# Kernel optimization log

Measured on AMD Instinct MI355X. Metric: run time of the kernel, lower is better.

The kernel has to match this reference:

```python
import jax, jax.numpy as jnp
import numpy as np

ROPE_BASE = 10000.0

def _rope_tables(T, head_dim, dtype):
    inv_freq = 1.0 / (ROPE_BASE ** (jnp.arange(0, head_dim, 2, dtype=jnp.float32) / head_dim))
    freqs = jnp.arange(T, dtype=jnp.float32)[:, None] * inv_freq[None, :]  # (T, hd/2)
    freqs = jnp.repeat(freqs, 2, axis=-1)  # (T, hd) interleaved (lucidrains-style)
    return jnp.cos(freqs).astype(dtype), jnp.sin(freqs).astype(dtype)

def _rotate_half(x):
    # interleaved pairs: (..., d) -> (-x2, x1) interleaved
    x = x.reshape(x.shape[:-1] + (-1, 2))
    x1, x2 = x[..., 0], x[..., 1]
    return jnp.stack((-x2, x1), axis=-1).reshape(x.shape[:-2] + (-1,))

def _apply_rope(x, cos, sin):
    # x: (B, H, T, hd); cos/sin: (T, hd)
    return x * cos[None, None] + _rotate_half(x) * sin[None, None]

def setup_inputs() -> dict:
    key = jax.random.key(0)
    k1, k2, k3 = jax.random.split(key, 3)
    B, T, C = 4, 2048, 1024
    x = jax.random.normal(k1, (B, T, C), dtype=jnp.float32)
    W_attn = jax.random.normal(k2, (C, 3 * C), dtype=jnp.float32) * 0.02
    W_proj = jax.random.normal(k3, (C, C), dtype=jnp.float32) * 0.02
    return {"x": x, "W_attn": W_attn, "W_proj": W_proj}

def reference(x, W_attn, W_proj):
    B, T, C = x.shape
    n_head = 16
    hd = C // n_head
    qkv = x @ W_attn  # (B, T, 3C)
    q, k, v = jnp.split(qkv, 3, axis=-1)
    # (B, T, H, hd) -> (B, H, T, hd)
    q = q.reshape(B, T, n_head, hd).transpose(0, 2, 1, 3)
    k = k.reshape(B, T, n_head, hd).transpose(0, 2, 1, 3)
    v = v.reshape(B, T, n_head, hd).transpose(0, 2, 1, 3)
    cos, sin = _rope_tables(T, hd, x.dtype)
    q = _apply_rope(q, cos, sin)
    k = _apply_rope(k, cos, sin)
    att = jnp.einsum('bhqd,bhkd->bhqk', q, k) * (1.0 / jnp.sqrt(jnp.array(hd, dtype=x.dtype)))
    causal = jnp.tril(jnp.ones((T, T), dtype=bool))
    att = jnp.where(causal[None, None], att, jnp.array(-jnp.inf, dtype=att.dtype))
    att = jax.nn.softmax(att, axis=-1)
    y = jnp.einsum('bhqk,bhkd->bhqd', att, v)
    y = y.transpose(0, 2, 1, 3).reshape(B, T, C)
    return y @ W_proj
```

## Files before the change

kernel.cpp:

```cpp
#include <hip/hip_runtime.h>
#include <hip/hip_bf16.h>
#include <math.h>

#define BB 4
#define TT 2048
#define CC 1024
#define NH 16
#define HD 64
#define C3 3072
#define LDK 72

#define QSCALE 0.18033688011112042f

typedef __attribute__((ext_vector_type(8))) short bf16x8;
typedef __attribute__((ext_vector_type(4))) float f32x4;

__device__ __forceinline__ void gload_lds16(const __hip_bfloat16* g, __hip_bfloat16* s) {
    __builtin_amdgcn_global_load_lds((const __attribute__((address_space(1))) void*)g,
                                     (__attribute__((address_space(3))) void*)s, 16, 0, 0);
}

__global__ __launch_bounds__(256) void rope_tables(float2* __restrict__ tab) {
    int idx = blockIdx.x * 256 + threadIdx.x;
    int t = idx >> 5;
    int p = idx & 31;
    float invf = exp2f((float)p * (-13.287712379549449f / 32.0f));
    float ang = (float)t * invf;
    float s, c;
    sincosf(ang, &s, &c);
    tab[idx] = make_float2(c, s);
}

__global__ __launch_bounds__(256) void cast_bf16x8(const float* __restrict__ X,
                                                   __hip_bfloat16* __restrict__ Y) {
    size_t i = ((size_t)blockIdx.x * 256 + threadIdx.x) * 8;
    float4 a = *(const float4*)(X + i);
    float4 b = *(const float4*)(X + i + 4);
    __align__(16) __hip_bfloat16 tmp[8];
    tmp[0] = __float2bfloat16(a.x);
    tmp[1] = __float2bfloat16(a.y);
    tmp[2] = __float2bfloat16(a.z);
    tmp[3] = __float2bfloat16(a.w);
    tmp[4] = __float2bfloat16(b.x);
    tmp[5] = __float2bfloat16(b.y);
    tmp[6] = __float2bfloat16(b.z);
    tmp[7] = __float2bfloat16(b.w);
    *(bf16x8*)(Y + i) = *(bf16x8*)tmp;
}

__global__ __launch_bounds__(256) void wtrans(const float* __restrict__ W,
                                              __hip_bfloat16* __restrict__ Wt,
                                              int K, int N) {
    __shared__ float st[64][65];
    const int n0 = blockIdx.x * 64;
    const int k0 = blockIdx.y * 64;
    const int tid = threadIdx.x;
    const int r = tid >> 4;
    const int c4 = (tid & 15) * 4;
#pragma unroll
    for (int p = 0; p < 4; ++p) {
        int k = p * 16 + r;
        float4 v = *(const float4*)(W + (size_t)(k0 + k) * N + n0 + c4);
        st[c4 + 0][k] = v.x;
        st[c4 + 1][k] = v.y;
        st[c4 + 2][k] = v.z;
        st[c4 + 3][k] = v.w;
    }
    __syncthreads();
    const int rr = tid >> 3;
    const int cc = (tid & 7) * 8;
#pragma unroll
    for (int p = 0; p < 2; ++p) {
        int n = p * 32 + rr;
        __align__(16) __hip_bfloat16 tmp[8];
#pragma unroll
        for (int j = 0; j < 8; ++j) tmp[j] = __float2bfloat16(st[n][cc + j]);
        *(bf16x8*)(Wt + (size_t)(n0 + n) * K + k0 + cc) = *(bf16x8*)tmp;
    }
}

#define CA0 0
#define CA1 1
#define CB0 2
#define CB1 3

#define BAR() __builtin_amdgcn_s_barrier()
#define SB0() __builtin_amdgcn_sched_barrier(0)
#define WAIT_LGKM0() do { asm volatile("s_waitcnt lgkmcnt(0)" ::: "memory"); SB0(); } while (0)
#define WAIT_VM4()   do { asm volatile("s_waitcnt vmcnt(4)" ::: "memory");  SB0(); } while (0)

#define CLAMP_TS(x) ((x) < NTILE ? (x) : (x) - 2)

#define STAGE(gbase, h, ts, buf, cid) do {                                            \
    const __hip_bfloat16* _s = (gbase) + (size_t)((h) * 128 + w * 16) * K + (ts) * 64; \
    __hip_bfloat16* _d = &lds[buf][cid][w * 1024];                                    \
    gload_lds16(_s, _d);                                                              \
    gload_lds16(_s + 32, _d + 512);                                                   \
} while (0)

#define FRAGP(buf, cid, rowsub, ks)                                                   \
    ((const bf16x8*)((const char*)&lds[buf][cid][0] +                                 \
        (((rowsub) * 2 + (ks)) << 10) + (l16 << 6) + swzoff))

#define READ_A(buf, mi) do {                                                          \
    _Pragma("unroll") for (int _m = 0; _m < 4; ++_m)                                  \
    _Pragma("unroll") for (int _k = 0; _k < 2; ++_k)                                  \
        af[_m][_k] = *FRAGP(buf, wm, (mi) * 4 + _m, _k);                              \
} while (0)

#define READ_B(buf, ni) do {                                                          \
    _Pragma("unroll") for (int _n = 0; _n < 2; ++_n)                                  \
    _Pragma("unroll") for (int _k = 0; _k < 2; ++_k)                                  \
        bfr[(ni) * 2 + _n][_k] =                                                      \
            *FRAGP(buf, 2 + (wn >> 1), (wn & 1) * 4 + (ni) * 2 + _n, _k);             \
} while (0)

#define MFMA_Q(mb, nb) do {                                                           \
    __builtin_amdgcn_s_setprio(1);                                                    \
    _Pragma("unroll") for (int _m = 0; _m < 4; ++_m)                                  \
    _Pragma("unroll") for (int _n = 0; _n < 2; ++_n)                                  \
    _Pragma("unroll") for (int _k = 0; _k < 2; ++_k)                                  \
        acc[(mb) * 4 + _m][(nb) * 2 + _n] = __builtin_amdgcn_mfma_f32_16x16x32_bf16(  \
            af[_m][_k], bfr[(nb) * 2 + _n][_k], acc[(mb) * 4 + _m][(nb) * 2 + _n],    \
            0, 0, 0);                                                                 \
    __builtin_amdgcn_s_setprio(0);                                                    \
} while (0)

#define HALF_ITER(BUF, T12, B12, T34, B34) do {                                       \
                                                                 \
    READ_A(BUF, 0);                                                                   \
    READ_B(BUF, 0);                                                                   \
    STAGE(Bb, 1, CLAMP_TS(T12), B12, CB1);                                            \
    BAR(); WAIT_LGKM0();                                                              \
    MFMA_Q(0, 0);                                                                     \
    BAR();                                                                            \
                                                                 \
    READ_B(BUF, 1);                                                                   \
    STAGE(Ab, 1, CLAMP_TS(T12), B12, CA1);                                            \
    BAR(); WAIT_LGKM0();                                                              \
    MFMA_Q(0, 1);                                                                     \
    BAR();                                                                            \
                                                                 \
    READ_A(BUF, 1);                                                                   \
    STAGE(Bb, 0, CLAMP_TS(T34), B34, CB0);                                            \
    BAR(); WAIT_LGKM0();                                                              \
    MFMA_Q(1, 0);                                                                     \
    BAR();                                                                            \
                                                                 \
    STAGE(Ab, 0, CLAMP_TS(T34), B34, CA0);                                            \
    BAR(); WAIT_LGKM0();                                                              \
    MFMA_Q(1, 1);                                                                     \
    WAIT_VM4();                                                                       \
    BAR(); SB0();                                                                     \
} while (0)

#define GEMM256_BODY                                                                  \
    __shared__ __align__(16) __hip_bfloat16 lds[2][4][8192];             \
    const int tid = threadIdx.x;                                                      \
    const int w = tid >> 6;                                                           \
    const int lane = tid & 63;                                                        \
    const int l16 = lane & 15;                                                        \
    const int quad = lane >> 4;                                                       \
    const int wm = w >> 2;                                                            \
    const int wn = w & 3;                                                             \
    const int swzoff = ((quad * 8) ^ ((l16 & 8) << 1)) << 1;                          \
    const int bm0 = blockIdx.y * 256;                                                 \
    const int bn0 = blockIdx.x * 256;                                                 \
    const int NTILE = K >> 6;                                                         \
    const size_t laneOff = (size_t)(lane >> 2) * K +                                  \
                           (((lane & 3) * 8) ^ ((lane >> 5) << 4));                   \
    const __hip_bfloat16* Ab = A + (size_t)bm0 * K + laneOff;                         \
    const __hip_bfloat16* Bb = Bt + (size_t)bn0 * K + laneOff;                        \
    f32x4 acc[8][4] = {};                                                             \
             \
    STAGE(Bb, 0, 0, 0, CB0);                                                          \
    STAGE(Ab, 0, 0, 0, CA0);                                                          \
    STAGE(Bb, 1, 0, 0, CB1);                                                          \
    STAGE(Ab, 1, 0, 0, CA1);                                                          \
    STAGE(Bb, 0, 1, 1, CB0);                                                          \
    STAGE(Ab, 0, 1, 1, CA0);                                                          \
    WAIT_VM4();                                                                       \
    BAR(); SB0();                                                                     \
    for (int it = 0; it < NTILE / 2; ++it) {                                          \
        const int t = it * 2;                                                         \
        bf16x8 af[4][2], bfr[4][2];                                                   \
        HALF_ITER(0, t + 1, 1, t + 2, 0);                                             \
        HALF_ITER(1, t + 2, 0, t + 3, 1);                                             \
    }

__global__ __launch_bounds__(512) void gemm256_qkv_rope(const __hip_bfloat16* __restrict__ A,
                                                        const __hip_bfloat16* __restrict__ Bt,
                                                        const float2* __restrict__ tab,
                                                        __hip_bfloat16* __restrict__ C,
                                                        int M, int N, int K) {
    GEMM256_BODY

    if (bn0 < 2048) {
        const float qsc = (bn0 < 1024) ? QSCALE : 1.0f;
        const float sgn = (l16 & 1) ? 1.0f : -1.0f;
#pragma unroll
        for (int mt = 0; mt < 8; ++mt) {
            int row = bm0 + wm * 128 + mt * 16 + quad * 4;
#pragma unroll
            for (int nt = 0; nt < 4; ++nt) {
                int col = bn0 + wn * 64 + nt * 16 + l16;
                int p2 = nt * 8 + (l16 >> 1);
#pragma unroll
                for (int r = 0; r < 4; ++r) {
                    float own = acc[mt][nt][r];
                    float part = __shfl_xor(own, 1);
                    int trow = (row + r) & (TT - 1);
                    float2 cs = tab[(trow << 5) + p2];
                    float res = (own * cs.x + sgn * part * cs.y) * qsc;
                    C[(size_t)(row + r) * N + col] = __float2bfloat16(res);
                }
            }
        }
    } else {
#pragma unroll
        for (int mt = 0; mt < 8; ++mt) {
            int row = bm0 + wm * 128 + mt * 16 + quad * 4;
#pragma unroll
            for (int nt = 0; nt < 4; ++nt) {
                int col = bn0 + wn * 64 + nt * 16 + l16;
#pragma unroll
                for (int r = 0; r < 4; ++r)
                    C[(size_t)(row + r) * N + col] = __float2bfloat16(acc[mt][nt][r]);
            }
        }
    }
}

__global__ __launch_bounds__(512) void gemm256_f32(const __hip_bfloat16* __restrict__ A,
                                                   const __hip_bfloat16* __restrict__ Bt,
                                                   float* __restrict__ C,
                                                   int M, int N, int K) {
    GEMM256_BODY
#pragma unroll
    for (int mt = 0; mt < 8; ++mt) {
        int row = bm0 + wm * 128 + mt * 16 + quad * 4;
#pragma unroll
        for (int nt = 0; nt < 4; ++nt) {
            int col = bn0 + wn * 64 + nt * 16 + l16;
#pragma unroll
            for (int r = 0; r < 4; ++r)
                C[(size_t)(row + r) * N + col] = acc[mt][nt][r];
        }
    }
}

__global__ __launch_bounds__(256) void vtranspose(const __hip_bfloat16* __restrict__ qkvb,
                                                  __hip_bfloat16* __restrict__ vtb) {
    __shared__ __align__(16) __hip_bfloat16 st[64][LDK];
    const int bh = blockIdx.x >> 5;
    const int tt = blockIdx.x & 31;
    const int b = bh >> 4;
    const int h = bh & 15;
    const int tid = threadIdx.x;
    const int row = tid >> 3;
    const int col8 = (tid & 7) * 8;

#pragma unroll
    for (int pass = 0; pass < 2; ++pass) {
        int t = pass * 32 + row;
        *(bf16x8*)(&st[t][col8]) =
            *(const bf16x8*)(qkvb + ((size_t)(b * TT + tt * 64 + t)) * C3 + 2 * CC + h * HD + col8);
    }
    __syncthreads();
#pragma unroll
    for (int pass = 0; pass < 2; ++pass) {
        int d = pass * 32 + row;
        __align__(16) __hip_bfloat16 tmp[8];
#pragma unroll
        for (int j = 0; j < 8; ++j) tmp[j] = st[col8 + j][d];
        *(bf16x8*)(vtb + ((size_t)bh * HD + d) * TT + tt * 64 + col8) = *(bf16x8*)tmp;
    }
}

__global__ __launch_bounds__(256) void attn_mfma5(const __hip_bfloat16* __restrict__ qkvb,
                                                  const __hip_bfloat16* __restrict__ vtb,
                                                  __hip_bfloat16* __restrict__ y) {
    __shared__ __align__(16) __hip_bfloat16 Kb[2][64 * 64];
    __shared__ __align__(16) __hip_bfloat16 Vb[2][64 * 64];
    __shared__ __align__(16) __hip_bfloat16 Ps[4][2][16 * 72];

    const int tid = threadIdx.x;
    const int w = tid >> 6;
    const int lane = tid & 63;
    const int l16 = lane & 15;
    const int quad = lane >> 4;
    const int swz = l16 & 7;

    const int bh = blockIdx.x >> 3;
    const int pr = blockIdx.x & 7;
    const int b = bh >> 4;
    const int h = bh & 15;

    const int sr = (lane >> 3) & 7;
    const int sc = lane & 7;
    const int klog = (sc ^ sr) * 8;

    const __hip_bfloat16* kbase = qkvb + (size_t)b * TT * C3 + CC + h * HD + klog;
    const __hip_bfloat16* vbase = vtb + (size_t)bh * HD * TT + klog;

#pragma unroll
    for (int seg = 0; seg < 2; ++seg) {
        const int qblk = (seg == 0) ? (15 - pr) : pr;
        const int qb = qblk * 128;
        const int jtmax = 2 * qblk + 1;
        const int qn0 = qb + w * 32;
        const int qn1 = qn0 + 16;

        bf16x8 qf[2][2];
#pragma unroll
        for (int qt = 0; qt < 2; ++qt) {
            const __hip_bfloat16* qp = qkvb + (size_t)(b * TT + qn0 + qt * 16 + l16) * C3 + h * HD;
            qf[qt][0] = *(const bf16x8*)(qp + quad * 8);
            qf[qt][1] = *(const bf16x8*)(qp + 32 + quad * 8);
        }

        f32x4 O[2][4] = {};
        float l_q[2] = {0.f, 0.f};

        __syncthreads();
#pragma unroll
        for (int half = 0; half < 2; ++half) {
            int kr = w * 16 + half * 8 + sr;
            gload_lds16(kbase + (size_t)kr * C3, Kb[0] + (w * 16 + half * 8) * 64);
            gload_lds16(vbase + (size_t)kr * TT, Vb[0] + (w * 16 + half * 8) * 64);
        }

        for (int jt = 0; jt <= jtmax; ++jt) {
            const int p = jt & 1;
            __syncthreads();

            if (jt < jtmax) {
                const int jn = jt + 1;
#pragma unroll
                for (int half = 0; half < 2; ++half) {
                    int kr = w * 16 + half * 8 + sr;
                    gload_lds16(kbase + (size_t)(jn * 64 + kr) * C3,
                                Kb[p ^ 1] + (w * 16 + half * 8) * 64);
                    gload_lds16(vbase + (size_t)kr * TT + jn * 64,
                                Vb[p ^ 1] + (w * 16 + half * 8) * 64);
                }
            }

            const bool sk0 = (jt * 64 > qn0 + 15);
            const bool sk1 = (jt * 64 > qn1 + 15);

            if (!sk1) {
                f32x4 St[2][4] = {};
#pragma unroll
                for (int ks = 0; ks < 2; ++ks) {
#pragma unroll
                    for (int mt = 0; mt < 4; ++mt) {
                        bf16x8 kf = *(const bf16x8*)(Kb[p] + (mt * 16 + l16) * 64 +
                                                     ((ks * 4 + quad) ^ swz) * 8);
                        St[0][mt] = __builtin_amdgcn_mfma_f32_16x16x32_bf16(kf, qf[0][ks], St[0][mt], 0, 0, 0);
                        St[1][mt] = __builtin_amdgcn_mfma_f32_16x16x32_bf16(kf, qf[1][ks], St[1][mt], 0, 0, 0);
                    }
                }

#pragma unroll
                for (int qt = 0; qt < 2; ++qt) {
                    const bool skq = qt == 0 ? sk0 : sk1;
                    if (skq) continue;
                    const int qn = qt == 0 ? qn0 : qn1;
                    if (jt * 64 + 63 > qn) {
#pragma unroll
                        for (int mt = 0; mt < 4; ++mt) {
#pragma unroll
                            for (int r = 0; r < 4; ++r) {
                                int key = jt * 64 + mt * 16 + quad * 4 + r;
                                if (key > qn + l16) St[qt][mt][r] = -__builtin_inff();
                            }
                        }
                    }
                    float sum = 0.f;
#pragma unroll
                    for (int mt = 0; mt < 4; ++mt) {
                        float e0 = exp2f(St[qt][mt][0]);
                        float e1 = exp2f(St[qt][mt][1]);
                        float e2 = exp2f(St[qt][mt][2]);
                        float e3 = exp2f(St[qt][mt][3]);
                        sum += (e0 + e1) + (e2 + e3);
                        union { uint2 u; __hip_bfloat162 h[2]; } up;
                        up.h[0] = __float22bfloat162_rn(make_float2(e0, e1));
                        up.h[1] = __float22bfloat162_rn(make_float2(e2, e3));
                        *(uint2*)(&Ps[w][qt][l16 * 72 + mt * 16 + quad * 4]) = up.u;
                    }
                    l_q[qt] += sum;
                }

                bf16x8 vf[4][2];
#pragma unroll
                for (int dt = 0; dt < 4; ++dt) {
                    vf[dt][0] = *(const bf16x8*)(Vb[p] + (dt * 16 + l16) * 64 + ((quad) ^ swz) * 8);
                    vf[dt][1] = *(const bf16x8*)(Vb[p] + (dt * 16 + l16) * 64 + ((4 + quad) ^ swz) * 8);
                }
#pragma unroll
                for (int qt = 0; qt < 2; ++qt) {
                    const bool skq = qt == 0 ? sk0 : sk1;
                    if (skq) continue;
                    bf16x8 pa0 = *(const bf16x8*)(&Ps[w][qt][l16 * 72 + quad * 8]);
                    bf16x8 pa1 = *(const bf16x8*)(&Ps[w][qt][l16 * 72 + 32 + quad * 8]);
#pragma unroll
                    for (int dt = 0; dt < 4; ++dt) {
                        O[qt][dt] = __builtin_amdgcn_mfma_f32_16x16x32_bf16(pa0, vf[dt][0], O[qt][dt], 0, 0, 0);
                        O[qt][dt] = __builtin_amdgcn_mfma_f32_16x16x32_bf16(pa1, vf[dt][1], O[qt][dt], 0, 0, 0);
                    }
                }
            }
        }

#pragma unroll
        for (int qt = 0; qt < 2; ++qt) {
            float l2 = l_q[qt];
            l2 += __shfl_xor(l2, 16);
            l2 += __shfl_xor(l2, 32);
            float lO[4];
#pragma unroll
            for (int r = 0; r < 4; ++r) lO[r] = 1.0f / __shfl(l2, quad * 4 + r);
            const int qbase = qn0 + qt * 16 + quad * 4;
#pragma unroll
            for (int dt = 0; dt < 4; ++dt) {
#pragma unroll
                for (int r = 0; r < 4; ++r) {
                    y[(size_t)(b * TT + qbase + r) * CC + h * HD + dt * 16 + l16] =
                        __float2bfloat16(O[qt][dt][r] * lO[r]);
                }
            }
        }
    }
}

extern "C" void kernel_launch(void* const* d_in, const int* in_sizes, int n_in,
                              void* d_out, int out_size, void* d_ws, size_t ws_size,
                              hipStream_t stream) {
    const float* x      = (const float*)d_in[0];
    const float* W_attn = (const float*)d_in[1];
    const float* W_proj = (const float*)d_in[2];
    float* out = (float*)d_out;

    const size_t NBT = (size_t)BB * TT;
    __hip_bfloat16* xb   = (__hip_bfloat16*)d_ws;
    __hip_bfloat16* qkvb = xb + NBT * CC;
    __hip_bfloat16* vtb  = qkvb + NBT * C3;
    __hip_bfloat16* Wab  = vtb + NBT * CC;
    __hip_bfloat16* Wpb  = Wab + (size_t)CC * C3;
    float2* tab          = (float2*)(Wpb + (size_t)CC * CC);
    __hip_bfloat16* yb   = xb;

    const int M = BB * TT;

    rope_tables<<<dim3(TT * 32 / 256), 256, 0, stream>>>(tab);
    cast_bf16x8<<<dim3((int)(NBT * CC / 2048)), 256, 0, stream>>>(x, xb);
    wtrans<<<dim3(C3 / 64, CC / 64), 256, 0, stream>>>(W_attn, Wab, CC, C3);
    wtrans<<<dim3(CC / 64, CC / 64), 256, 0, stream>>>(W_proj, Wpb, CC, CC);

    gemm256_qkv_rope<<<dim3(C3 / 256, M / 256), 512, 0, stream>>>(xb, Wab, tab, qkvb, M, C3, CC);

    vtranspose<<<dim3(BB * NH * (TT / 64)), 256, 0, stream>>>(qkvb, vtb);

    attn_mfma5<<<dim3(BB * NH * 8), 256, 0, stream>>>(qkvb, vtb, yb);

    gemm256_f32<<<dim3(CC / 256, M / 256), 512, 0, stream>>>(yb, Wpb, out, M, CC, CC);
}
```

Baseline: 292.3 us.

## Triple-buffer K/V tiles in attention with explicit vmcnt waits and MFMA priority

The attention kernel moves from double to triple buffering of K and V tiles in LDS, prefetching two tiles ahead. It replaces the full __syncthreads with an explicit vmcnt wait plus barrier, so only the older loads must land before compute. It also raises wave priority with s_setprio around the MFMA blocks. The aim is to hide global-to-LDS latency better, at the cost of extra LDS (48 KB for K/V) that may reduce occupancy.

New measurement: 290.7 us. No clear change (-0.5%).

```diff
diff --git a/kernel.cpp b/kernel.cpp
--- a/kernel.cpp
+++ b/kernel.cpp
@@ -88,6 +88,7 @@
 #define SB0() __builtin_amdgcn_sched_barrier(0)
 #define WAIT_LGKM0() do { asm volatile("s_waitcnt lgkmcnt(0)" ::: "memory"); SB0(); } while (0)
 #define WAIT_VM4()   do { asm volatile("s_waitcnt vmcnt(4)" ::: "memory");  SB0(); } while (0)
+#define WAIT_VM0()   do { asm volatile("s_waitcnt vmcnt(0)" ::: "memory");  SB0(); } while (0)
 
 #define CLAMP_TS(x) ((x) < NTILE ? (x) : (x) - 2)
 
@@ -277,11 +278,11 @@
     }
 }
 
-__global__ __launch_bounds__(256) void attn_mfma5(const __hip_bfloat16* __restrict__ qkvb,
+__global__ __launch_bounds__(256) void attn_mfma6(const __hip_bfloat16* __restrict__ qkvb,
                                                   const __hip_bfloat16* __restrict__ vtb,
                                                   __hip_bfloat16* __restrict__ y) {
-    __shared__ __align__(16) __hip_bfloat16 Kb[2][64 * 64];
-    __shared__ __align__(16) __hip_bfloat16 Vb[2][64 * 64];
+    __shared__ __align__(16) __hip_bfloat16 Kb[3][64 * 64];
+    __shared__ __align__(16) __hip_bfloat16 Vb[3][64 * 64];
     __shared__ __align__(16) __hip_bfloat16 Ps[4][2][16 * 72];
 
     const int tid = threadIdx.x;
@@ -303,6 +304,17 @@
     const __hip_bfloat16* kbase = qkvb + (size_t)b * TT * C3 + CC + h * HD + klog;
     const __hip_bfloat16* vbase = vtb + (size_t)bh * HD * TT + klog;
 
+#define ATTN_STAGE(t, bidx) do {                                                  \
+    _Pragma("unroll")                                                             \
+    for (int half = 0; half < 2; ++half) {                                        \
+        int kr = w * 16 + half * 8 + sr;                                          \
+        gload_lds16(kbase + (size_t)((t) * 64 + kr) * C3,                         \
+                    Kb[bidx] + (w * 16 + half * 8) * 64);                         \
+        gload_lds16(vbase + (size_t)kr * TT + (t) * 64,                           \
+                    Vb[bidx] + (w * 16 + half * 8) * 64);                         \
+    }                                                                             \
+} while (0)
+
 #pragma unroll
     for (int seg = 0; seg < 2; ++seg) {
         const int qblk = (seg == 0) ? (15 - pr) : pr;
@@ -323,44 +335,39 @@
         float l_q[2] = {0.f, 0.f};
 
         __syncthreads();
-#pragma unroll
-        for (int half = 0; half < 2; ++half) {
-            int kr = w * 16 + half * 8 + sr;
-            gload_lds16(kbase + (size_t)kr * C3, Kb[0] + (w * 16 + half * 8) * 64);
-            gload_lds16(vbase + (size_t)kr * TT, Vb[0] + (w * 16 + half * 8) * 64);
-        }
-
+        ATTN_STAGE(0, 0);
+        ATTN_STAGE(1, 1);
+
+        int bcur = 0;
         for (int jt = 0; jt <= jtmax; ++jt) {
-            const int p = jt & 1;
-            __syncthreads();
-
-            if (jt < jtmax) {
-                const int jn = jt + 1;
-#pragma unroll
-                for (int half = 0; half < 2; ++half) {
-                    int kr = w * 16 + half * 8 + sr;
-                    gload_lds16(kbase + (size_t)(jn * 64 + kr) * C3,
-                                Kb[p ^ 1] + (w * 16 + half * 8) * 64);
-                    gload_lds16(vbase + (size_t)kr * TT + jn * 64,
-                                Vb[p ^ 1] + (w * 16 + half * 8) * 64);
-                }
+            if (jt < jtmax) { WAIT_VM4(); } else { WAIT_VM0(); }
+            BAR(); SB0();
+
+            if (jt + 2 <= jtmax) {
+                const int bs = (bcur >= 1) ? (bcur - 1) : 2;
+                ATTN_STAGE(jt + 2, bs);
             }
+
+            const __hip_bfloat16* Kp = Kb[bcur];
+            const __hip_bfloat16* Vp = Vb[bcur];
 
             const bool sk0 = (jt * 64 > qn0 + 15);
             const bool sk1 = (jt * 64 > qn1 + 15);
 
             if (!sk1) {
                 f32x4 St[2][4] = {};
+                __builtin_amdgcn_s_setprio(1);
 #pragma unroll
                 for (int ks = 0; ks < 2; ++ks) {
 #pragma unroll
                     for (int mt = 0; mt < 4; ++mt) {
-                        bf16x8 kf = *(const bf16x8*)(Kb[p] + (mt * 16 + l16) * 64 +
+                        bf16x8 kf = *(const bf16x8*)(Kp + (mt * 16 + l16) * 64 +
                                                      ((ks * 4 + quad) ^ swz) * 8);
                         St[0][mt] = __builtin_amdgcn_mfma_f32_16x16x32_bf16(kf, qf[0][ks], St[0][mt], 0, 0, 0);
                         St[1][mt] = __builtin_amdgcn_mfma_f32_16x16x32_bf16(kf, qf[1][ks], St[1][mt], 0, 0, 0);
                     }
                 }
+                __builtin_amdgcn_s_setprio(0);
 
 #pragma unroll
                 for (int qt = 0; qt < 2; ++qt) {
@@ -396,9 +403,10 @@
                 bf16x8 vf[4][2];
 #pragma unroll
                 for (int dt = 0; dt < 4; ++dt) {
-                    vf[dt][0] = *(const bf16x8*)(Vb[p] + (dt * 16 + l16) * 64 + ((quad) ^ swz) * 8);
-                    vf[dt][1] = *(const bf16x8*)(Vb[p] + (dt * 16 + l16) * 64 + ((4 + quad) ^ swz) * 8);
-                }
+                    vf[dt][0] = *(const bf16x8*)(Vp + (dt * 16 + l16) * 64 + ((quad) ^ swz) * 8);
+                    vf[dt][1] = *(const bf16x8*)(Vp + (dt * 16 + l16) * 64 + ((4 + quad) ^ swz) * 8);
+                }
+                __builtin_amdgcn_s_setprio(1);
 #pragma unroll
                 for (int qt = 0; qt < 2; ++qt) {
                     const bool skq = qt == 0 ? sk0 : sk1;
@@ -411,7 +419,10 @@
                         O[qt][dt] = __builtin_amdgcn_mfma_f32_16x16x32_bf16(pa1, vf[dt][1], O[qt][dt], 0, 0, 0);
                     }
                 }
+                __builtin_amdgcn_s_setprio(0);
             }
+
+            bcur = (bcur == 2) ? 0 : bcur + 1;
         }
 
 #pragma unroll
@@ -433,6 +444,7 @@
             }
         }
     }
+#undef ATTN_STAGE
 }
 
 extern "C" void kernel_launch(void* const* d_in, const int* in_sizes, int n_in,
@@ -463,7 +475,7 @@
 
     vtranspose<<<dim3(BB * NH * (TT / 64)), 256, 0, stream>>>(qkvb, vtb);
 
-    attn_mfma5<<<dim3(BB * NH * 8), 256, 0, stream>>>(qkvb, vtb, yb);
+    attn_mfma6<<<dim3(BB * NH * 8), 256, 0, stream>>>(qkvb, vtb, yb);
 
     gemm256_f32<<<dim3(CC / 256, M / 256), 512, 0, stream>>>(yb, Wpb, out, M, CC, CC);
 }
```
